# Kernel tuning notes

Hardware: AMD Instinct MI355X
Metric: run time of the kernel (lower is better)

The kernel has to match this reference:

```python
import jax, jax.numpy as jnp
import numpy as np

N = 50000      # nodes
F_IN = 1024    # raw feature dim
D = 64         # student_dim = hidden_dim * compression_ratio
P = 3          # number of meta-paths
E = 1600000    # edges per meta-path adjacency (avg degree 32)


def setup_inputs() -> dict:
    key = jax.random.key(0)
    ks = jax.random.split(key, 10)
    feats = jax.random.normal(ks[0], (N, F_IN), jnp.float32)
    rows = jax.random.randint(ks[1], (P, E), 0, N, dtype=jnp.int32)
    cols = jax.random.randint(ks[2], (P, E), 0, N, dtype=jnp.int32)
    # normalized-adjacency-like positive edge weights
    vals = jax.random.uniform(ks[3], (P, E), jnp.float32) / 32.0
    # fc_list[0]: Linear(F_IN -> D), xavier_normal gain=1.414
    W0 = jax.random.normal(ks[4], (D, F_IN), jnp.float32) * 0.05
    b0 = jnp.zeros((D,), jnp.float32)
    # P GCN linear layers (D -> D, no bias) + GCN bias params
    Wg = jax.random.normal(ks[5], (P, D, D), jnp.float32) * 0.17
    bg = jnp.zeros((P, D), jnp.float32)
    # PReLU alpha (torch default init 0.25, one scalar per GCN)
    alpha = jnp.full((P,), 0.25, jnp.float32)
    # Attention: Linear(D -> D) and att vector [1, D]
    Wa = jax.random.normal(ks[6], (D, D), jnp.float32) * 0.17
    ba = jnp.zeros((D,), jnp.float32)
    att = jax.random.normal(ks[7], (1, D), jnp.float32) * 0.17
    return dict(feats=feats, rows=rows, cols=cols, vals=vals, W0=W0, b0=b0,
                Wg=Wg, bg=bg, alpha=alpha, Wa=Wa, ba=ba, att=att)


def reference(feats, rows, cols, vals, W0, b0, Wg, bg, alpha, Wa, ba, att):
    # h = elu(fc_list[0](feats))  (feat_drop = 0 -> identity)
    h = jax.nn.elu(feats @ W0.T + b0)                       # [N, D]
    embeds = []
    for i in range(P):
        s = h @ Wg[i].T                                     # [N, D]
        # sparse adj (COO) @ s : out[r] += v * s[c]
        msg = vals[i][:, None] * s[cols[i]]                 # [E, D]
        out = jax.ops.segment_sum(msg, rows[i], num_segments=N)
        out = out + bg[i]
        embeds.append(jnp.where(out > 0, out, alpha[i] * out))  # PReLU
    emb = jnp.stack(embeds)                                 # [P, N, D]
    # Attention over views: beta_i = att . mean_n tanh(fc(emb_i))
    sp = jnp.tanh(jnp.einsum('pnd,ed->pne', emb, Wa) + ba).mean(axis=1)  # [P, D]
    beta = jax.nn.softmax(sp @ att[0])                      # [P]
    z_mp = jnp.einsum('p,pnd->nd', beta, emb)               # [N, D]
    return z_mp
```

## Files before the change

kernel.cpp:

```cpp
#include <hip/hip_runtime.h>
#include <hip/hip_bf16.h>

#define N_NODES 50000
#define F_IN    1024
#define DD      64
#define PP      3
#define EE      1600000
#define NPC     98
#define CCAP    17664

typedef __attribute__((ext_vector_type(8))) short short8v;
typedef __attribute__((ext_vector_type(4))) float floatx4;

__device__ inline float bfl(uint u) { return __uint_as_float(u << 16); }
__device__ inline float bfh(uint u) { return __uint_as_float(u & 0xffff0000u); }
__device__ inline uint cvtpk2(float a, float b) {
    __hip_bfloat162 h = __float22bfloat162_rn(make_float2(a, b));
    return *(uint*)&h;
}
__device__ inline ushort f2bf(float x) {
    __hip_bfloat16 h = __float2bfloat16(x);
    return *(ushort*)&h;
}

__global__ __launch_bounds__(256) void split_weights(const float* __restrict__ W0,
                                                     const float* __restrict__ Wg,
                                                     ushort* __restrict__ W0h,
                                                     ushort* __restrict__ Wgh)
{
    int i = blockIdx.x * 256 + threadIdx.x;
    if (i < 64 * 1024) W0h[i] = f2bf(W0[i]);
    int j = i - 64 * 1024;
    if (j >= 0 && j < PP * 64 * 64) Wgh[j] = f2bf(Wg[j]);
}

__global__ __launch_bounds__(256) void gemm1_mfma(const float* __restrict__ feats,
                                                  const ushort* __restrict__ W0h,
                                                  const float* __restrict__ b0,
                                                  ushort* __restrict__ h_bf)
{
    __shared__ ushort Ah[64 * 64];
    __shared__ ushort Bh[64 * 64];
    const int t = threadIdx.x;
    const int w = t >> 6, lane = t & 63;
    const int row0 = blockIdx.x * 64;
    const int l15 = lane & 15, l4 = lane >> 4;

    floatx4 acc[4] = {};

    for (int kc = 0; kc < 16; ++kc) {
        #pragma unroll
        for (int rep = 0; rep < 4; ++rep) {
            int idx = rep * 256 + t;
            int r = idx >> 4, c4 = idx & 15;
            int gr = row0 + r; if (gr >= N_NODES) gr = N_NODES - 1;
            float4 v = *(const float4*)&feats[(size_t)gr * F_IN + kc * 64 + c4 * 4];
            int unit = (c4 >> 1) ^ (r & 7);
            int base = r * 64 + unit * 8 + (c4 & 1) * 4;
            *(uint2*)&Ah[base] = make_uint2(cvtpk2(v.x, v.y), cvtpk2(v.z, v.w));
        }
        #pragma unroll
        for (int rep = 0; rep < 2; ++rep) {
            int idx = rep * 256 + t;
            int c = idx >> 3, u8 = idx & 7;
            uint4 vh = *(const uint4*)&W0h[(size_t)c * F_IN + kc * 64 + u8 * 8];
            int unit = u8 ^ (c & 7);
            *(uint4*)&Bh[c * 64 + unit * 8] = vh;
        }
        __syncthreads();
        #pragma unroll
        for (int ks = 0; ks < 2; ++ks) {
            int arow = w * 16 + l15;
            int au = (ks * 4 + l4) ^ (arow & 7);
            short8v ah = *(short8v*)&Ah[arow * 64 + au * 8];
            #pragma unroll
            for (int cf = 0; cf < 4; ++cf) {
                int bcol = cf * 16 + l15;
                int bu = (ks * 4 + l4) ^ (bcol & 7);
                short8v bh = *(short8v*)&Bh[bcol * 64 + bu * 8];
                acc[cf] = __builtin_amdgcn_mfma_f32_16x16x32_bf16(ah, bh, acc[cf], 0, 0, 0);
            }
        }
        __syncthreads();
    }

    #pragma unroll
    for (int cf = 0; cf < 4; ++cf) {
        int col = cf * 16 + l15;
        #pragma unroll
        for (int r = 0; r < 4; ++r) {
            int gr = row0 + w * 16 + l4 * 4 + r;
            if (gr < N_NODES) {
                float x = acc[cf][r] + b0[col];
                x = x > 0.f ? x : (__expf(x) - 1.f);
                h_bf[(size_t)gr * 64 + col] = f2bf(x);
            }
        }
    }
}

__global__ __launch_bounds__(256) void gemm_s(const ushort* __restrict__ h_bf,
                                              const ushort* __restrict__ Wgh,
                                              ushort* __restrict__ s_all)
{
    __shared__ ushort Ah[64 * 64];
    __shared__ ushort Bh[64 * 64];
    const int t = threadIdx.x;
    const int w = t >> 6, lane = t & 63;
    const int p = blockIdx.y;
    const int row0 = blockIdx.x * 64;
    const int l15 = lane & 15, l4 = lane >> 4;

    #pragma unroll
    for (int rep = 0; rep < 2; ++rep) {
        int idx = rep * 256 + t;
        int r = idx >> 3, u8 = idx & 7;
        int gr = row0 + r; if (gr >= N_NODES) gr = N_NODES - 1;
        int unit = u8 ^ (r & 7);
        *(uint4*)&Ah[r * 64 + unit * 8] = *(const uint4*)&h_bf[(size_t)gr * 64 + u8 * 8];
        *(uint4*)&Bh[r * 64 + unit * 8] = *(const uint4*)&Wgh[(size_t)p * 4096 + idx * 8];
    }
    __syncthreads();

    floatx4 acc[4] = {};
    #pragma unroll
    for (int ks = 0; ks < 2; ++ks) {
        int arow = w * 16 + l15;
        int au = (ks * 4 + l4) ^ (arow & 7);
        short8v ah = *(short8v*)&Ah[arow * 64 + au * 8];
        #pragma unroll
        for (int cf = 0; cf < 4; ++cf) {
            int bcol = cf * 16 + l15;
            int bu = (ks * 4 + l4) ^ (bcol & 7);
            short8v bh = *(short8v*)&Bh[bcol * 64 + bu * 8];
            acc[cf] = __builtin_amdgcn_mfma_f32_16x16x32_bf16(ah, bh, acc[cf], 0, 0, 0);
        }
    }

    ushort* sp = s_all + (size_t)p * N_NODES * 64;
    #pragma unroll
    for (int cf = 0; cf < 4; ++cf) {
        int col = cf * 16 + l15;
        #pragma unroll
        for (int r = 0; r < 4; ++r) {
            int gr = row0 + w * 16 + l4 * 4 + r;
            if (gr < N_NODES)
                sp[(size_t)gr * 64 + col] = f2bf(acc[cf][r]);
        }
    }
}

__global__ __launch_bounds__(256) void part1(const int*   __restrict__ rows,
                                             const int*   __restrict__ cols,
                                             const float* __restrict__ vals,
                                             int*   __restrict__ pcur3,
                                             uint2* __restrict__ coarsebuf)
{
    __shared__ uint2 stage[2560];
    __shared__ uint2 sorted[2560];
    __shared__ int cnt[128];
    __shared__ int sc[128];
    __shared__ int curb[128];
    __shared__ int gbase[128];
    const int t = threadIdx.x;
    const int path = blockIdx.y;
    const size_t ebase = (size_t)path * EE + (size_t)blockIdx.x * 2560;
    int* pcur = pcur3 + path * NPC;
    uint2* cb = coarsebuf + (size_t)path * NPC * CCAP;

    if (t < 128) { cnt[t] = 0; curb[t] = 0; }
    __syncthreads();

    #pragma unroll
    for (int it = 0; it < 10; ++it) {
        int e = it * 256 + t;
        int r = rows[ebase + e];
        int c = cols[ebase + e];
        float v = vals[ebase + e];
        int bin = r >> 9, rl = r & 511;
        stage[e] = make_uint2((uint)c | ((uint)rl << 16) | ((uint)bin << 25),
                              __float_as_uint(v));
        atomicAdd(&cnt[bin], 1);
    }
    __syncthreads();

    if (t < 128) sc[t] = cnt[t];
    __syncthreads();
    #pragma unroll
    for (int o = 1; o < 128; o <<= 1) {
        int v = (t < 128 && t >= o) ? sc[t - o] : 0;
        __syncthreads();
        if (t < 128 && t >= o) sc[t] += v;
        __syncthreads();
    }

    if (t < NPC) gbase[t] = atomicAdd(&pcur[t], cnt[t]);
    __syncthreads();

    #pragma unroll
    for (int it = 0; it < 10; ++it) {
        uint2 e = stage[it * 256 + t];
        int bin = e.x >> 25;
        int loc = (sc[bin] - cnt[bin]) + atomicAdd(&curb[bin], 1);
        sorted[loc] = e;
    }
    __syncthreads();

    #pragma unroll
    for (int it = 0; it < 10; ++it) {
        int i = it * 256 + t;
        uint2 e = sorted[i];
        int bin = e.x >> 25;
        int g = gbase[bin] + (i - (sc[bin] - cnt[bin]));
        if (g < CCAP) cb[(size_t)bin * CCAP + g] = e;
    }
}

__global__ __launch_bounds__(512) void sort2(const uint2* __restrict__ coarsebuf,
                                             const int*   __restrict__ pcur3,
                                             uint* __restrict__ sortpk,
                                             int* __restrict__ rowbeg3,
                                             int* __restrict__ rowend3)
{
    __shared__ int hist[512];
    __shared__ int cur[512];
    const int t = threadIdx.x;
    const int c = blockIdx.x, path = blockIdx.y;
    const int n = min(pcur3[path * NPC + c], CCAP);
    const size_t slabbase = ((size_t)path * NPC + c) * CCAP;
    const uint2* src = coarsebuf + slabbase;

    hist[t] = 0;
    __syncthreads();

    for (int i = t; i < n; i += 512)
        atomicAdd(&hist[(src[i].x >> 16) & 511], 1);
    __syncthreads();

    int c0 = hist[t];
    __syncthreads();
    #pragma unroll
    for (int o = 1; o < 512; o <<= 1) {
        int v = (t >= o) ? hist[t - o] : 0;
        __syncthreads();
        hist[t] += v;
        __syncthreads();
    }
    int excl = hist[t] - c0;
    cur[t] = excl;
    int gr = c * 512 + t;
    if (gr < N_NODES) {
        rowbeg3[path * N_NODES + gr] = (int)(slabbase + excl);
        rowend3[path * N_NODES + gr] = (int)(slabbase + excl + c0);
    }
    __syncthreads();

    for (int i = t; i < n; i += 512) {
        uint2 e = src[i];
        int rl = (e.x >> 16) & 511;
        int pos = atomicAdd(&cur[rl], 1);
        sortpk[slabbase + pos] = (e.x & 0xffffu) |
                                 ((uint)f2bf(__uint_as_float(e.y)) << 16);
    }
}

__global__ __launch_bounds__(256) void spmm_gather(const uint*   __restrict__ sortpk,
                                                   const int*    __restrict__ rowbeg3,
                                                   const int*    __restrict__ rowend3,
                                                   const ushort* __restrict__ s_all,
                                                   const float*  __restrict__ bg,
                                                   const float*  __restrict__ alpha,
                                                   ushort* __restrict__ emb)
{
    const int path = blockIdx.y;
    const int wid = blockIdx.x * 4 + (threadIdx.x >> 6);
    const int lane = threadIdx.x & 63;
    const int dq = lane & 7;
    const int slot = lane >> 3;
    const int e0 = rowbeg3[path * N_NODES + wid];
    const int e1 = rowend3[path * N_NODES + wid];
    const ushort* s_p = s_all + (size_t)path * N_NODES * 64;

    float acc[8] = {};
    for (int e = e0; e < e1; e += 32) {
        int ea = e + slot, eb = ea + 8, ec = ea + 16, ed = ea + 24;
        uint pka = (ea < e1) ? sortpk[ea] : 0u;
        uint pkb = (eb < e1) ? sortpk[eb] : 0u;
        uint pkc = (ec < e1) ? sortpk[ec] : 0u;
        uint pkd = (ed < e1) ? sortpk[ed] : 0u;
        uint4 ga = *(const uint4*)&s_p[(size_t)(pka & 0xffffu) * 64 + dq * 8];
        uint4 gb = *(const uint4*)&s_p[(size_t)(pkb & 0xffffu) * 64 + dq * 8];
        uint4 gc = *(const uint4*)&s_p[(size_t)(pkc & 0xffffu) * 64 + dq * 8];
        uint4 gd = *(const uint4*)&s_p[(size_t)(pkd & 0xffffu) * 64 + dq * 8];
        float va = bfh(pka);
        float vb = bfh(pkb);
        float vc = bfh(pkc);
        float vd = bfh(pkd);
        acc[0] += va * bfl(ga.x); acc[1] += va * bfh(ga.x);
        acc[2] += va * bfl(ga.y); acc[3] += va * bfh(ga.y);
        acc[4] += va * bfl(ga.z); acc[5] += va * bfh(ga.z);
        acc[6] += va * bfl(ga.w); acc[7] += va * bfh(ga.w);
        acc[0] += vb * bfl(gb.x); acc[1] += vb * bfh(gb.x);
        acc[2] += vb * bfl(gb.y); acc[3] += vb * bfh(gb.y);
        acc[4] += vb * bfl(gb.z); acc[5] += vb * bfh(gb.z);
        acc[6] += vb * bfl(gb.w); acc[7] += vb * bfh(gb.w);
        acc[0] += vc * bfl(gc.x); acc[1] += vc * bfh(gc.x);
        acc[2] += vc * bfl(gc.y); acc[3] += vc * bfh(gc.y);
        acc[4] += vc * bfl(gc.z); acc[5] += vc * bfh(gc.z);
        acc[6] += vc * bfl(gc.w); acc[7] += vc * bfh(gc.w);
        acc[0] += vd * bfl(gd.x); acc[1] += vd * bfh(gd.x);
        acc[2] += vd * bfl(gd.y); acc[3] += vd * bfh(gd.y);
        acc[4] += vd * bfl(gd.z); acc[5] += vd * bfh(gd.z);
        acc[6] += vd * bfl(gd.w); acc[7] += vd * bfh(gd.w);
    }
    #pragma unroll
    for (int j = 0; j < 8; ++j) {
        acc[j] += __shfl_xor(acc[j], 8);
        acc[j] += __shfl_xor(acc[j], 16);
        acc[j] += __shfl_xor(acc[j], 32);
    }

    if (slot == 0) {
        const float al = alpha[path];
        const float* bgp = bg + path * 64;
        float x[8];
        #pragma unroll
        for (int j = 0; j < 8; ++j) {
            float v = acc[j] + bgp[dq * 8 + j];
            x[j] = v > 0.f ? v : al * v;
        }
        uint4 wv;
        wv.x = cvtpk2(x[0], x[1]);
        wv.y = cvtpk2(x[2], x[3]);
        wv.z = cvtpk2(x[4], x[5]);
        wv.w = cvtpk2(x[6], x[7]);
        *(uint4*)&emb[((size_t)path * N_NODES + wid) * 64 + dq * 8] = wv;
    }
}

__global__ __launch_bounds__(256) void postproc(const ushort* __restrict__ emb,
                                                const float* __restrict__ Wa,
                                                const float* __restrict__ ba,
                                                float* __restrict__ sp)
{
    __shared__ float Ws[64][64];
    __shared__ float As[64][64];
    __shared__ float red[16][64];
    const int t  = threadIdx.x;
    const int tx = t & 15;
    const int ty = t >> 4;
    const int nb = (N_NODES + 63) >> 6;
    const int p  = blockIdx.x / nb;
    const int tb = blockIdx.x % nb;
    const int row0 = tb * 64;
    const ushort* embp = emb + (size_t)p * N_NODES * 64;

    #pragma unroll
    for (int rep = 0; rep < 4; ++rep) {
        int id = rep * 1024 + t * 4;
        int e  = id >> 6;
        int k4 = id & 63;
        float4 wv = *(const float4*)&Wa[id];
        Ws[k4+0][e] = wv.x; Ws[k4+1][e] = wv.y;
        Ws[k4+2][e] = wv.z; Ws[k4+3][e] = wv.w;
    }
    #pragma unroll
    for (int rep = 0; rep < 2; ++rep) {
        int idx = rep * 256 + t;
        int m  = idx >> 3;
        int d8 = idx & 7;
        int gr = row0 + m;
        int gr2 = gr < N_NODES ? gr : N_NODES - 1;
        uint4 xv = *(const uint4*)&embp[(size_t)gr2 * 64 + d8 * 8];
        As[d8*8+0][m] = bfl(xv.x); As[d8*8+1][m] = bfh(xv.x);
        As[d8*8+2][m] = bfl(xv.y); As[d8*8+3][m] = bfh(xv.y);
        As[d8*8+4][m] = bfl(xv.z); As[d8*8+5][m] = bfh(xv.z);
        As[d8*8+6][m] = bfl(xv.w); As[d8*8+7][m] = bfh(xv.w);
    }
    __syncthreads();

    float acc[4][4] = {};
    #pragma unroll 8
    for (int kk = 0; kk < 64; ++kk) {
        float4 a4 = *(const float4*)&As[kk][ty * 4];
        float4 b4 = *(const float4*)&Ws[kk][tx * 4];
        float av[4] = {a4.x, a4.y, a4.z, a4.w};
        float bv[4] = {b4.x, b4.y, b4.z, b4.w};
        #pragma unroll
        for (int i = 0; i < 4; ++i)
            #pragma unroll
            for (int j = 0; j < 4; ++j)
                acc[i][j] += av[i] * bv[j];
    }

    float colsum[4] = {0.f, 0.f, 0.f, 0.f};
    #pragma unroll
    for (int i = 0; i < 4; ++i) {
        int gr = row0 + ty * 4 + i;
        if (gr < N_NODES) {
            #pragma unroll
            for (int j = 0; j < 4; ++j)
                colsum[j] += tanhf(acc[i][j] + ba[tx * 4 + j]);
        }
    }
    #pragma unroll
    for (int j = 0; j < 4; ++j) red[ty][tx * 4 + j] = colsum[j];
    __syncthreads();
    if (t < 64) {
        float ssum = 0.f;
        #pragma unroll
        for (int g = 0; g < 16; ++g) ssum += red[g][t];
        unsafeAtomicAdd(&sp[p * 64 + t], ssum);
    }
}

__global__ void beta_kernel(const float* __restrict__ sp,
                            const float* __restrict__ att,
                            float* __restrict__ beta)
{
    int lane = threadIdx.x;
    float w[PP];
    #pragma unroll
    for (int p = 0; p < PP; ++p) {
        float x = sp[p * 64 + lane] * (1.0f / (float)N_NODES) * att[lane];
        #pragma unroll
        for (int off = 32; off; off >>= 1) x += __shfl_down(x, off);
        w[p] = __shfl(x, 0);
    }
    if (lane == 0) {
        float mx = fmaxf(w[0], fmaxf(w[1], w[2]));
        float e0 = __expf(w[0] - mx);
        float e1 = __expf(w[1] - mx);
        float e2 = __expf(w[2] - mx);
        float s = e0 + e1 + e2;
        beta[0] = e0 / s; beta[1] = e1 / s; beta[2] = e2 / s;
    }
}

__global__ __launch_bounds__(256) void combine(const ushort* __restrict__ emb,
                                               const float* __restrict__ beta,
                                               float* __restrict__ out)
{
    const float b0 = beta[0], b1 = beta[1], b2 = beta[2];
    const size_t tot = (size_t)N_NODES * 64;
    size_t i = ((size_t)blockIdx.x * 256 + threadIdx.x) * 8;
    if (i < tot) {
        uint4 e0 = *(const uint4*)&emb[i];
        uint4 e1 = *(const uint4*)&emb[tot + i];
        uint4 e2 = *(const uint4*)&emb[2 * tot + i];
        float o[8];
        o[0] = b0*bfl(e0.x) + b1*bfl(e1.x) + b2*bfl(e2.x);
        o[1] = b0*bfh(e0.x) + b1*bfh(e1.x) + b2*bfh(e2.x);
        o[2] = b0*bfl(e0.y) + b1*bfl(e1.y) + b2*bfl(e2.y);
        o[3] = b0*bfh(e0.y) + b1*bfh(e1.y) + b2*bfh(e2.y);
        o[4] = b0*bfl(e0.z) + b1*bfl(e1.z) + b2*bfl(e2.z);
        o[5] = b0*bfh(e0.z) + b1*bfh(e1.z) + b2*bfh(e2.z);
        o[6] = b0*bfl(e0.w) + b1*bfl(e1.w) + b2*bfl(e2.w);
        o[7] = b0*bfh(e0.w) + b1*bfh(e1.w) + b2*bfh(e2.w);
        *(float4*)&out[i]     = make_float4(o[0], o[1], o[2], o[3]);
        *(float4*)&out[i + 4] = make_float4(o[4], o[5], o[6], o[7]);
    }
}

extern "C" void kernel_launch(void* const* d_in, const int* in_sizes, int n_in,
                              void* d_out, int out_size, void* d_ws, size_t ws_size,
                              hipStream_t stream)
{
    const float* feats = (const float*)d_in[0];
    const int*   rows  = (const int*)  d_in[1];
    const int*   cols  = (const int*)  d_in[2];
    const float* vals  = (const float*)d_in[3];
    const float* W0    = (const float*)d_in[4];
    const float* b0    = (const float*)d_in[5];
    const float* Wg    = (const float*)d_in[6];
    const float* bg    = (const float*)d_in[7];
    const float* alpha = (const float*)d_in[8];
    const float* Wa    = (const float*)d_in[9];
    const float* ba    = (const float*)d_in[10];
    const float* att   = (const float*)d_in[11];
    float* out = (float*)d_out;

    const size_t ND = (size_t)N_NODES * 64;
    char* base = (char*)d_ws;
    ushort* emb    = (ushort*)base;              base += 3 * ND * 2;
    ushort* h_bf   = (ushort*)base;              base += ND * 2;
    ushort* s_all  = (ushort*)base;              base += 3 * ND * 2;
    ushort* W0h    = (ushort*)base;              base += 64 * 1024 * 2;
    ushort* Wgh    = (ushort*)base;              base += PP * 64 * 64 * 2;
    int*    pcur3  = (int*)base;                 base += PP * NPC * 4;
    float*  sp     = (float*)base;               base += 192 * 4;
    float*  beta   = (float*)base;               base += 64 * 4;
    int*    rowbeg3 = (int*)base;                base += PP * N_NODES * 4;
    int*    rowend3 = (int*)base;                base += PP * N_NODES * 4;
    base = (char*)(((size_t)base + 255) & ~(size_t)255);
    uint2*  coarsebuf = (uint2*)base;            base += (size_t)PP * NPC * CCAP * 8;
    uint*   sortpk    = (uint*)base;             base += (size_t)PP * NPC * CCAP * 4;

    hipMemsetAsync(pcur3, 0, (PP * NPC + 192) * sizeof(int), stream);

    split_weights<<<(64 * 1024 + PP * 64 * 64 + 255) / 256, 256, 0, stream>>>(
        W0, Wg, W0h, Wgh);

    gemm1_mfma<<<782, 256, 0, stream>>>(feats, W0h, b0, h_bf);
    gemm_s<<<dim3(782, 3), 256, 0, stream>>>(h_bf, Wgh, s_all);

    part1<<<dim3(EE / 2560, 3), 256, 0, stream>>>(rows, cols, vals, pcur3, coarsebuf);
    sort2<<<dim3(NPC, 3), 512, 0, stream>>>(coarsebuf, pcur3, sortpk, rowbeg3, rowend3);
    spmm_gather<<<dim3(N_NODES / 4, 3), 256, 0, stream>>>(
        sortpk, rowbeg3, rowend3, s_all, bg, alpha, emb);

    postproc<<<3 * 782, 256, 0, stream>>>(emb, Wa, ba, sp);
    beta_kernel<<<1, 64, 0, stream>>>(sp, att, beta);
    combine<<<(int)((ND / 8 + 255) / 256), 256, 0, stream>>>(emb, beta, out);
}
```

Before: 318.7 us.

## Fuse feature GEMM with per-path GCN GEMMs and split gather into column halves

Folds the per-path h@Wg GEMM into the first GEMM kernel, keeping the ELU output tile in shared memory so h never goes to global memory and one launch is removed. The per-path s tensor is now stored as two 32-column halves. The SpMM gather runs one slice per half, so each half table is smaller and more cache-friendly for random gathers. The cost is that the edge list and row offsets are read twice, and each wave gathers only two edges per iteration.

```diff
diff --git a/kernel.cpp b/kernel.cpp
--- a/kernel.cpp
+++ b/kernel.cpp
@@ -34,10 +34,11 @@
     if (j >= 0 && j < PP * 64 * 64) Wgh[j] = f2bf(Wg[j]);
 }
 
-__global__ __launch_bounds__(256) void gemm1_mfma(const float* __restrict__ feats,
-                                                  const ushort* __restrict__ W0h,
-                                                  const float* __restrict__ b0,
-                                                  ushort* __restrict__ h_bf)
+__global__ __launch_bounds__(256) void gemm1_fused(const float* __restrict__ feats,
+                                                   const ushort* __restrict__ W0h,
+                                                   const float* __restrict__ b0,
+                                                   const ushort* __restrict__ Wgh,
+                                                   ushort* __restrict__ s_all)
 {
     __shared__ ushort Ah[64 * 64];
     __shared__ ushort Bh[64 * 64];
@@ -89,64 +90,52 @@
         int col = cf * 16 + l15;
         #pragma unroll
         for (int r = 0; r < 4; ++r) {
-            int gr = row0 + w * 16 + l4 * 4 + r;
-            if (gr < N_NODES) {
-                float x = acc[cf][r] + b0[col];
-                x = x > 0.f ? x : (__expf(x) - 1.f);
-                h_bf[(size_t)gr * 64 + col] = f2bf(x);
+            int row = w * 16 + l4 * 4 + r;
+            float x = acc[cf][r] + b0[col];
+            x = x > 0.f ? x : (__expf(x) - 1.f);
+            int u = (col >> 3) ^ (row & 7);
+            Ah[row * 64 + u * 8 + (col & 7)] = f2bf(x);
+        }
+    }
+    __syncthreads();
+
+    for (int p = 0; p < PP; ++p) {
+        #pragma unroll
+        for (int rep = 0; rep < 2; ++rep) {
+            int idx = rep * 256 + t;
+            int r = idx >> 3, u8 = idx & 7;
+            int unit = u8 ^ (r & 7);
+            *(uint4*)&Bh[r * 64 + unit * 8] = *(const uint4*)&Wgh[(size_t)p * 4096 + idx * 8];
+        }
+        __syncthreads();
+
+        floatx4 sacc[4] = {};
+        #pragma unroll
+        for (int ks = 0; ks < 2; ++ks) {
+            int arow = w * 16 + l15;
+            int au = (ks * 4 + l4) ^ (arow & 7);
+            short8v ah = *(short8v*)&Ah[arow * 64 + au * 8];
+            #pragma unroll
+            for (int cf = 0; cf < 4; ++cf) {
+                int bcol = cf * 16 + l15;
+                int bu = (ks * 4 + l4) ^ (bcol & 7);
+                short8v bh = *(short8v*)&Bh[bcol * 64 + bu * 8];
+                sacc[cf] = __builtin_amdgcn_mfma_f32_16x16x32_bf16(ah, bh, sacc[cf], 0, 0, 0);
             }
         }
-    }
-}
-
-__global__ __launch_bounds__(256) void gemm_s(const ushort* __restrict__ h_bf,
-                                              const ushort* __restrict__ Wgh,
-                                              ushort* __restrict__ s_all)
-{
-    __shared__ ushort Ah[64 * 64];
-    __shared__ ushort Bh[64 * 64];
-    const int t = threadIdx.x;
-    const int w = t >> 6, lane = t & 63;
-    const int p = blockIdx.y;
-    const int row0 = blockIdx.x * 64;
-    const int l15 = lane & 15, l4 = lane >> 4;
-
-    #pragma unroll
-    for (int rep = 0; rep < 2; ++rep) {
-        int idx = rep * 256 + t;
-        int r = idx >> 3, u8 = idx & 7;
-        int gr = row0 + r; if (gr >= N_NODES) gr = N_NODES - 1;
-        int unit = u8 ^ (r & 7);
-        *(uint4*)&Ah[r * 64 + unit * 8] = *(const uint4*)&h_bf[(size_t)gr * 64 + u8 * 8];
-        *(uint4*)&Bh[r * 64 + unit * 8] = *(const uint4*)&Wgh[(size_t)p * 4096 + idx * 8];
-    }
-    __syncthreads();
-
-    floatx4 acc[4] = {};
-    #pragma unroll
-    for (int ks = 0; ks < 2; ++ks) {
-        int arow = w * 16 + l15;
-        int au = (ks * 4 + l4) ^ (arow & 7);
-        short8v ah = *(short8v*)&Ah[arow * 64 + au * 8];
         #pragma unroll
         for (int cf = 0; cf < 4; ++cf) {
-            int bcol = cf * 16 + l15;
-            int bu = (ks * 4 + l4) ^ (bcol & 7);
-            short8v bh = *(short8v*)&Bh[bcol * 64 + bu * 8];
-            acc[cf] = __builtin_amdgcn_mfma_f32_16x16x32_bf16(ah, bh, acc[cf], 0, 0, 0);
-        }
-    }
-
-    ushort* sp = s_all + (size_t)p * N_NODES * 64;
-    #pragma unroll
-    for (int cf = 0; cf < 4; ++cf) {
-        int col = cf * 16 + l15;
-        #pragma unroll
-        for (int r = 0; r < 4; ++r) {
-            int gr = row0 + w * 16 + l4 * 4 + r;
-            if (gr < N_NODES)
-                sp[(size_t)gr * 64 + col] = f2bf(acc[cf][r]);
-        }
+            int col = cf * 16 + l15;
+            int half = col >> 5, ci = col & 31;
+            ushort* sp = s_all + (size_t)(p * 2 + half) * N_NODES * 32;
+            #pragma unroll
+            for (int r = 0; r < 4; ++r) {
+                int gr = row0 + w * 16 + l4 * 4 + r;
+                if (gr < N_NODES)
+                    sp[(size_t)gr * 32 + ci] = f2bf(sacc[cf][r]);
+            }
+        }
+        __syncthreads();
     }
 }
 
@@ -272,30 +261,25 @@
                                                    const float*  __restrict__ alpha,
                                                    ushort* __restrict__ emb)
 {
-    const int path = blockIdx.y;
-    const int wid = blockIdx.x * 4 + (threadIdx.x >> 6);
+    const int slice = blockIdx.x / 12500;
+    const int path = slice >> 1, half = slice & 1;
+    const int wid = (blockIdx.x % 12500) * 4 + (threadIdx.x >> 6);
     const int lane = threadIdx.x & 63;
-    const int dq = lane & 7;
-    const int slot = lane >> 3;
+    const int dq = lane & 3;
+    const int slot = lane >> 2;
     const int e0 = rowbeg3[path * N_NODES + wid];
     const int e1 = rowend3[path * N_NODES + wid];
-    const ushort* s_p = s_all + (size_t)path * N_NODES * 64;
+    const ushort* s_p = s_all + (size_t)slice * N_NODES * 32;
 
     float acc[8] = {};
     for (int e = e0; e < e1; e += 32) {
-        int ea = e + slot, eb = ea + 8, ec = ea + 16, ed = ea + 24;
+        int ea = e + slot, eb = ea + 16;
         uint pka = (ea < e1) ? sortpk[ea] : 0u;
         uint pkb = (eb < e1) ? sortpk[eb] : 0u;
-        uint pkc = (ec < e1) ? sortpk[ec] : 0u;
-        uint pkd = (ed < e1) ? sortpk[ed] : 0u;
-        uint4 ga = *(const uint4*)&s_p[(size_t)(pka & 0xffffu) * 64 + dq * 8];
-        uint4 gb = *(const uint4*)&s_p[(size_t)(pkb & 0xffffu) * 64 + dq * 8];
-        uint4 gc = *(const uint4*)&s_p[(size_t)(pkc & 0xffffu) * 64 + dq * 8];
-        uint4 gd = *(const uint4*)&s_p[(size_t)(pkd & 0xffffu) * 64 + dq * 8];
+        uint4 ga = *(const uint4*)&s_p[(size_t)(pka & 0xffffu) * 32 + dq * 8];
+        uint4 gb = *(const uint4*)&s_p[(size_t)(pkb & 0xffffu) * 32 + dq * 8];
         float va = bfh(pka);
         float vb = bfh(pkb);
-        float vc = bfh(pkc);
-        float vd = bfh(pkd);
         acc[0] += va * bfl(ga.x); acc[1] += va * bfh(ga.x);
         acc[2] += va * bfl(ga.y); acc[3] += va * bfh(ga.y);
         acc[4] += va * bfl(ga.z); acc[5] += va * bfh(ga.z);
@@ -304,17 +288,10 @@
         acc[2] += vb * bfl(gb.y); acc[3] += vb * bfh(gb.y);
         acc[4] += vb * bfl(gb.z); acc[5] += vb * bfh(gb.z);
         acc[6] += vb * bfl(gb.w); acc[7] += vb * bfh(gb.w);
-        acc[0] += vc * bfl(gc.x); acc[1] += vc * bfh(gc.x);
-        acc[2] += vc * bfl(gc.y); acc[3] += vc * bfh(gc.y);
-        acc[4] += vc * bfl(gc.z); acc[5] += vc * bfh(gc.z);
-        acc[6] += vc * bfl(gc.w); acc[7] += vc * bfh(gc.w);
-        acc[0] += vd * bfl(gd.x); acc[1] += vd * bfh(gd.x);
-        acc[2] += vd * bfl(gd.y); acc[3] += vd * bfh(gd.y);
-        acc[4] += vd * bfl(gd.z); acc[5] += vd * bfh(gd.z);
-        acc[6] += vd * bfl(gd.w); acc[7] += vd * bfh(gd.w);
     }
     #pragma unroll
     for (int j = 0; j < 8; ++j) {
+        acc[j] += __shfl_xor(acc[j], 4);
         acc[j] += __shfl_xor(acc[j], 8);
         acc[j] += __shfl_xor(acc[j], 16);
         acc[j] += __shfl_xor(acc[j], 32);
@@ -322,7 +299,7 @@
 
     if (slot == 0) {
         const float al = alpha[path];
-        const float* bgp = bg + path * 64;
+        const float* bgp = bg + path * 64 + half * 32;
         float x[8];
         #pragma unroll
         for (int j = 0; j < 8; ++j) {
@@ -334,7 +311,7 @@
         wv.y = cvtpk2(x[2], x[3]);
         wv.z = cvtpk2(x[4], x[5]);
         wv.w = cvtpk2(x[6], x[7]);
-        *(uint4*)&emb[((size_t)path * N_NODES + wid) * 64 + dq * 8] = wv;
+        *(uint4*)&emb[((size_t)path * N_NODES + wid) * 64 + half * 32 + dq * 8] = wv;
     }
 }
 
@@ -483,7 +460,6 @@
     const size_t ND = (size_t)N_NODES * 64;
     char* base = (char*)d_ws;
     ushort* emb    = (ushort*)base;              base += 3 * ND * 2;
-    ushort* h_bf   = (ushort*)base;              base += ND * 2;
     ushort* s_all  = (ushort*)base;              base += 3 * ND * 2;
     ushort* W0h    = (ushort*)base;              base += 64 * 1024 * 2;
     ushort* Wgh    = (ushort*)base;              base += PP * 64 * 64 * 2;
@@ -501,12 +477,11 @@
     split_weights<<<(64 * 1024 + PP * 64 * 64 + 255) / 256, 256, 0, stream>>>(
         W0, Wg, W0h, Wgh);
 
-    gemm1_mfma<<<782, 256, 0, stream>>>(feats, W0h, b0, h_bf);
-    gemm_s<<<dim3(782, 3), 256, 0, stream>>>(h_bf, Wgh, s_all);
+    gemm1_fused<<<782, 256, 0, stream>>>(feats, W0h, b0, Wgh, s_all);
 
     part1<<<dim3(EE / 2560, 3), 256, 0, stream>>>(rows, cols, vals, pcur3, coarsebuf);
     sort2<<<dim3(NPC, 3), 512, 0, stream>>>(coarsebuf, pcur3, sortpk, rowbeg3, rowend3);
-    spmm_gather<<<dim3(N_NODES / 4, 3), 256, 0, stream>>>(
+    spmm_gather<<<6 * 12500, 256, 0, stream>>>(
         sortpk, rowbeg3, rowend3, s_all, bg, alpha, emb);
 
     postproc<<<3 * 782, 256, 0, stream>>>(emb, Wa, ba, sp);
```

Result: slower. 351.9 us (+10.4%).
